# Optimization experiments

Measured on AMD Instinct MI355X. Metric: run time of the kernel, lower is better.

The kernel has to match this reference:

```python
import jax, jax.numpy as jnp
import numpy as np

S, E, K, D = 20000, 10000, 128, 128   # students, exercises, knowledge, latent dim
N_EK, N_SE = 40000, 500000            # exercise-knowledge edges, student-exercise edges
B = 2048                              # extract batch size


def setup_inputs() -> dict:
    key = jax.random.key(0)
    ks = jax.random.split(key, 16)
    inp = {}
    # Embedding tables (xavier-ish scale)
    inp["stu_emb"] = jax.random.normal(ks[0], (S, D), jnp.float32) * 0.1
    inp["exer_emb"] = jax.random.normal(ks[1], (E, D), jnp.float32) * 0.1
    inp["kn_emb"] = jax.random.normal(ks[2], (K, D), jnp.float32) * 0.1
    inp["disc_emb"] = jax.random.normal(ks[3], (E, 1), jnp.float32) * 0.1
    # GraphLayer params, stacked over [fusion_layer=2, graph={k_from_e,e_from_k,s_from_e,e_from_s}]
    inp["GW"] = jax.random.normal(ks[4], (2, 4, D, D), jnp.float32) * (1.0 / np.sqrt(D))
    inp["Ga"] = jax.random.normal(ks[5], (2, 4, 2 * D), jnp.float32) * 0.1
    # Fusion attention fcs: idx 0=e_attn_fc1, 1=e_attn_fc2, 2=k_attn_fc3 (weight [2D], bias scalar)
    inp["Fw"] = jax.random.normal(ks[6], (2, 3, 2 * D), jnp.float32) * 0.1
    inp["Fb"] = jax.random.normal(ks[7], (2, 3), jnp.float32) * 0.1
    # q_mask (unused by extract, part of the signature)
    inp["q_mask"] = jax.random.bernoulli(ks[8], 0.03, (B, K)).astype(jnp.float32)
    inp["student_id"] = jax.random.randint(ks[9], (B,), 0, S, jnp.int32)
    inp["exercise_id"] = jax.random.randint(ks[10], (B,), 0, E, jnp.int32)
    # k_from_e graph: nodes = [exercises 0..E) ++ [knowledge E..E+K); edges exercise -> knowledge
    inp["ek_src"] = jax.random.randint(ks[11], (N_EK,), 0, E, jnp.int32)
    inp["ek_dst"] = E + jax.random.randint(ks[12], (N_EK,), 0, K, jnp.int32)
    # s_from_e graph: nodes = [exercises 0..E) ++ [students E..E+S); edges exercise -> student
    inp["se_src"] = jax.random.randint(ks[13], (N_SE,), 0, E, jnp.int32)
    inp["se_dst"] = E + jax.random.randint(ks[14], (N_SE,), 0, S, jnp.int32)
    return inp


def _graph_layer(h, W, a, src, dst, n):
    # GAT-style: z = h W; per-edge score a^T [z_src; z_dst]; segment softmax over dst; weighted sum of z_src.
    z = h @ W                                   # [n, D]
    zs, zd = z[src], z[dst]                     # [ne, D] gathers
    e = jnp.concatenate([zs, zd], axis=1) @ a   # [ne]
    emax = jax.ops.segment_max(e, dst, num_segments=n)
    emax = jnp.where(jnp.isfinite(emax), emax, 0.0)  # empty segments -> -inf -> 0
    ex = jnp.exp(e - emax[dst])
    den = jax.ops.segment_sum(ex, dst, num_segments=n)
    alpha = ex / jnp.where(den > 0, den, 1.0)[dst]
    return jax.ops.segment_sum(alpha[:, None] * zs, dst, num_segments=n)  # nodes w/o mail -> 0 (DGL semantics)


def _fusion(kn, ex, st, GWl, Gal, Fwl, Fbl, ek_src, ek_dst, se_src, se_dst):
    nek, nes = E + K, E + S
    ekg = jnp.concatenate([ex, kn], axis=0)
    kfe = _graph_layer(ekg, GWl[0], Gal[0], ek_src, ek_dst, nek)  # k_from_e
    efk = _graph_layer(ekg, GWl[1], Gal[1], ek_dst, ek_src, nek)  # e_from_k (reversed edges)
    esg = jnp.concatenate([ex, st], axis=0)
    ufe = _graph_layer(esg, GWl[2], Gal[2], se_src, se_dst, nes)  # s_from_e
    efu = _graph_layer(esg, GWl[3], Gal[3], se_dst, se_src, nes)  # e_from_s (reversed edges)
    # knowledge update: softmax over a single column == 1 (faithful to original)
    Dk = kfe[E:]
    s3 = jax.nn.softmax((jnp.concatenate([kn, Dk], axis=1) @ Fwl[2] + Fbl[2])[:, None], axis=1)
    kn2 = kn + s3[:, 0:1] * Dk
    # exercise update: 2-way softmax gate
    Bx, Cx = efk[:E], efu[:E]
    s1 = jnp.concatenate([ex, Bx], axis=1) @ Fwl[0] + Fbl[0]
    s2 = jnp.concatenate([ex, Cx], axis=1) @ Fwl[1] + Fbl[1]
    sc = jax.nn.softmax(jnp.stack([s1, s2], axis=1), axis=1)  # [E, 2]
    ex2 = ex + sc[:, 0:1] * Bx + sc[:, 1:2] * Cx
    st2 = st + ufe[E:]
    return kn2, ex2, st2


def reference(stu_emb, exer_emb, kn_emb, disc_emb, GW, Ga, Fw, Fb, q_mask,
              student_id, exercise_id, ek_src, ek_dst, se_src, se_dst):
    kn, ex, st = kn_emb, exer_emb, stu_emb
    for l in range(2):  # FusionLayer1, FusionLayer2
        kn, ex, st = _fusion(kn, ex, st, GW[l], Ga[l], Fw[l], Fb[l],
                             ek_src, ek_dst, se_src, se_dst)
    bs = st[student_id]            # [B, D]
    be = ex[exercise_id]           # [B, D]
    disc = disc_emb[exercise_id]   # [B, 1]
    # if_type == 'rcd': repeat(1,D).reshape(B,D,D) == broadcast along axis 1
    stu_ts = jnp.broadcast_to(bs[:, None, :], (B, D, D))
    exer_ts = jnp.broadcast_to(be[:, None, :], (B, D, D))
    kn_ts = jnp.broadcast_to(kn[None, :, :], (B, K, D))
    return (stu_ts, exer_ts, disc, kn_ts)
```

## Files before the change

kernel.cpp:

```cpp
#include <hip/hip_runtime.h>

#define S_N 20000
#define E_N 10000
#define K_N 128
#define D_N 128
#define NEK 40000
#define NSE 500000
#define B_N 2048

typedef __attribute__((ext_vector_type(8))) short bf16x8;
typedef __attribute__((ext_vector_type(4))) float f32x4;

__device__ __forceinline__ unsigned short f2bf(float f){
  unsigned int u = __float_as_uint(f);
  unsigned int r = u + 0x7FFFu + ((u >> 16) & 1u);
  return (unsigned short)(r >> 16);
}
__device__ __forceinline__ float bf2f(unsigned short h){
  return __uint_as_float(((unsigned int)h) << 16);
}

struct GS { const unsigned short* Ah; const unsigned short* Al;
            const unsigned short* Wh; const unsigned short* Wl;
            float* Z; int rows; };
struct SSet { const float* z; const float* p; const int* rowptr; const int* col;
              const float* base; float* out; int ndst; };
struct CSet { const int* cnt; int n; int* rp; int* cur; };

__global__ __launch_bounds__(256) void k_wprep(const float* __restrict__ GW, const float* __restrict__ Ga,
                                               unsigned short* __restrict__ wf, float* __restrict__ wa){
  int g = blockIdx.x;
  const float* W  = GW + (size_t)g*16384;
  const float* a1 = Ga + (size_t)g*256;
  unsigned short* whi = wf + (size_t)g*16384;
  unsigned short* wlo = wf + (size_t)(8+g)*16384;
  int t = threadIdx.x, l = t & 63;
  for(int pi = t>>6; pi < 32; pi += 4){
    int c2 = pi >> 2, kt = pi & 3;
    unsigned short h[8], lo[8];
    #pragma unroll
    for(int j=0;j<8;j++){
      int k = kt*32 + (l>>4)*8 + j;
      int c = c2*16 + (l&15);
      float f = W[(size_t)k*128 + c];
      unsigned short hb = f2bf(f);
      h[j] = hb; lo[j] = f2bf(f - bf2f(hb));
    }
    size_t off = ((size_t)pi*64 + l)*8;
    uint4 hv, lv;
    hv.x = (unsigned)h[0] | ((unsigned)h[1]<<16);  hv.y = (unsigned)h[2] | ((unsigned)h[3]<<16);
    hv.z = (unsigned)h[4] | ((unsigned)h[5]<<16);  hv.w = (unsigned)h[6] | ((unsigned)h[7]<<16);
    lv.x = (unsigned)lo[0] | ((unsigned)lo[1]<<16); lv.y = (unsigned)lo[2] | ((unsigned)lo[3]<<16);
    lv.z = (unsigned)lo[4] | ((unsigned)lo[5]<<16); lv.w = (unsigned)lo[6] | ((unsigned)lo[7]<<16);
    *(uint4*)(whi + off) = hv;
    *(uint4*)(wlo + off) = lv;
  }
  for(int k = t; k < 128; k += 256){
    float s = 0.f;
    const float* wr = W + (size_t)k*128;
    for(int c=0;c<128;c++) s += wr[c]*a1[c];
    wa[(size_t)g*128 + k] = s;
  }
}

__global__ __launch_bounds__(256) void k_cvt(const float* __restrict__ kn, const float* __restrict__ ex,
    const float* __restrict__ st,
    unsigned short* __restrict__ knb, unsigned short* __restrict__ exb, unsigned short* __restrict__ stb,
    const float* __restrict__ wa, int l4,
    float* __restrict__ Pefk, float* __restrict__ Pkfe, float* __restrict__ Pufe, float* __restrict__ Pefu){
  int w = (blockIdx.x*256 + threadIdx.x) >> 6;
  int lane = threadIdx.x & 63;
  const float* src; unsigned short *hi, *lo; int r;
  const float* wv1; const float* wv2 = nullptr; float *P1, *P2 = nullptr;
  if(w < K_N){ r = w; src = kn + (size_t)r*128; hi = knb; lo = knb + (size_t)K_N*128;
               wv1 = wa + (size_t)(l4+1)*128; P1 = Pefk; }
  else if(w < K_N + E_N){ r = w - K_N; src = ex + (size_t)r*128; hi = exb; lo = exb + (size_t)E_N*128;
               wv1 = wa + (size_t)(l4+0)*128; P1 = Pkfe;
               wv2 = wa + (size_t)(l4+2)*128; P2 = Pufe; }
  else { r = w - K_N - E_N; if(r >= S_N) return; src = st + (size_t)r*128; hi = stb; lo = stb + (size_t)S_N*128;
               wv1 = wa + (size_t)(l4+3)*128; P1 = Pefu; }
  float2 x = ((const float2*)src)[lane];
  float2 v1 = ((const float2*)wv1)[lane];
  float d1 = x.x*v1.x + x.y*v1.y;
  float d2 = 0.f;
  if(wv2){ float2 v2 = ((const float2*)wv2)[lane]; d2 = x.x*v2.x + x.y*v2.y; }
  #pragma unroll
  for(int off=1; off<64; off<<=1){ d1 += __shfl_xor(d1,off); d2 += __shfl_xor(d2,off); }
  if(lane==0){ P1[r] = expf(d1); if(P2) P2[r] = expf(d2); }
  unsigned short h0 = f2bf(x.x), h1 = f2bf(x.y);
  unsigned short l0 = f2bf(x.x - bf2f(h0)), l1 = f2bf(x.y - bf2f(h1));
  ((ushort2*)(hi + (size_t)r*128))[lane] = make_ushort2(h0,h1);
  ((ushort2*)(lo + (size_t)r*128))[lane] = make_ushort2(l0,l1);
}

#define GT0 4
#define GT1 317
#define GT2 942
#define GT3 1255
__global__ __launch_bounds__(256) void k_gemm(GS g0, GS g1, GS g2, GS g3){
  int b = blockIdx.x;
  GS g; int lt;
  if(b < GT0){ g = g0; lt = b; }
  else if(b < GT1){ g = g1; lt = b - GT0; }
  else if(b < GT2){ g = g2; lt = b - GT1; }
  else { g = g3; lt = b - GT2; }
  int l = threadIdx.x & 63, wv = threadIdx.x >> 6;
  int r0 = lt*32;
  bf16x8 bh[2][4], bl[2][4];
  #pragma unroll
  for(int cs=0; cs<2; cs++)
    #pragma unroll
    for(int kt=0; kt<4; kt++){
      size_t o = (((size_t)((wv*2+cs)*4 + kt))*64 + l)*8;
      bh[cs][kt] = *(const bf16x8*)(g.Wh + o);
      bl[cs][kt] = *(const bf16x8*)(g.Wl + o);
    }
  f32x4 acc[2][2];
  #pragma unroll
  for(int rs=0;rs<2;rs++)
    #pragma unroll
    for(int cs=0;cs<2;cs++) acc[rs][cs] = (f32x4){0.f,0.f,0.f,0.f};
  #pragma unroll
  for(int kt=0; kt<4; kt++){
    bf16x8 ah[2], al[2];
    #pragma unroll
    for(int rs=0; rs<2; rs++){
      size_t ao = ((size_t)(r0 + rs*16 + (l&15)))*128 + kt*32 + (l>>4)*8;
      ah[rs] = *(const bf16x8*)(g.Ah + ao);
      al[rs] = *(const bf16x8*)(g.Al + ao);
    }
    #pragma unroll
    for(int rs=0; rs<2; rs++)
      #pragma unroll
      for(int cs=0; cs<2; cs++){
        acc[rs][cs] = __builtin_amdgcn_mfma_f32_16x16x32_bf16(ah[rs], bh[cs][kt], acc[rs][cs], 0,0,0);
        acc[rs][cs] = __builtin_amdgcn_mfma_f32_16x16x32_bf16(ah[rs], bl[cs][kt], acc[rs][cs], 0,0,0);
        acc[rs][cs] = __builtin_amdgcn_mfma_f32_16x16x32_bf16(al[rs], bh[cs][kt], acc[rs][cs], 0,0,0);
      }
  }
  #pragma unroll
  for(int rs=0; rs<2; rs++)
    #pragma unroll
    for(int cs=0; cs<2; cs++){
      int cb = (wv<<5) + (cs<<4) + (l&15);
      #pragma unroll
      for(int j=0;j<4;j++){
        int rr = r0 + rs*16 + ((l>>4)<<2) + j;
        if(rr < g.rows) g.Z[(size_t)rr*128 + cb] = acc[rs][cs][j];
      }
    }
}

__global__ __launch_bounds__(256) void k_hist(const int* __restrict__ eks, const int* __restrict__ ekd,
      const int* __restrict__ ses, const int* __restrict__ sed,
      int* c_eke, int* c_ekk, int* c_see, int* c_ses){
  int i = blockIdx.x*256 + threadIdx.x;
  if(i < NEK){ atomicAdd(c_eke + eks[i], 1); atomicAdd(c_ekk + (ekd[i]-E_N), 1); }
  if(i < NSE){ atomicAdd(c_see + ses[i], 1); atomicAdd(c_ses + (sed[i]-E_N), 1); }
}

__global__ __launch_bounds__(1024) void k_scan(CSet c0, CSet c1, CSet c2, CSet c3){
  CSet c = c0;
  if(blockIdx.x==1) c=c1; else if(blockIdx.x==2) c=c2; else if(blockIdx.x==3) c=c3;
  __shared__ int part[1024];
  int t = threadIdx.x;
  int n = c.n;
  int chunk = (n + 1023) >> 10;
  int b0 = t * chunk;
  int s = 0;
  for(int i=0;i<chunk;i++){ int idx=b0+i; if(idx<n) s += c.cnt[idx]; }
  part[t] = s;
  __syncthreads();
  for(int off=1; off<1024; off<<=1){
    int v = (t>=off) ? part[t-off] : 0;
    __syncthreads();
    part[t] += v;
    __syncthreads();
  }
  int run = t ? part[t-1] : 0;
  for(int i=0;i<chunk;i++){
    int idx=b0+i;
    if(idx<n){ int cc = c.cnt[idx]; c.rp[idx]=run; c.cur[idx]=run; run += cc; }
  }
  if(t==0) c.rp[n] = part[1023];
}

__global__ __launch_bounds__(256) void k_fill(const int* __restrict__ eks, const int* __restrict__ ekd,
      const int* __restrict__ ses, const int* __restrict__ sed,
      int* u_eke, int* u_ekk, int* u_see, int* u_ses,
      int* o_eke, int* o_ekk, int* o_see, int* o_ses){
  int i = blockIdx.x*256 + threadIdx.x;
  if(i < NEK){
    int a = eks[i], b = ekd[i];
    int pos = atomicAdd(u_eke + a, 1);        o_eke[pos] = b;
    int pos2 = atomicAdd(u_ekk + (b-E_N), 1); o_ekk[pos2] = a;
  }
  if(i < NSE){
    int a = ses[i], b = sed[i];
    int pos = atomicAdd(u_see + a, 1);        o_see[pos] = b;
    int pos2 = atomicAdd(u_ses + (b-E_N), 1); o_ses[pos2] = a;
  }
}

#define SB1 2500
#define SB2 5000
#define SB3 10000
#define SB4 10128
__global__ __launch_bounds__(256) void k_seg(SSet s0, SSet s1, SSet s2, SSet s3){
  __shared__ float4 red[4][32];
  __shared__ float redd[4];
  int b = blockIdx.x;
  int lane = threadIdx.x & 63, wid = threadIdx.x >> 6;
  int half = lane >> 5, l32 = lane & 31;
  SSet s; int row, str, stride; bool multi = false;
  if(b < SB1){ s = s0; row = b*4 + wid; }
  else if(b < SB2){ s = s1; row = (b-SB1)*4 + wid; }
  else if(b < SB3){ s = s2; row = (b-SB2)*4 + wid; }
  else { s = s3; row = b - SB3; multi = true; }
  if(!multi){ str = half; stride = 2; }
  else      { str = wid*2 + half; stride = 8; }
  if(row >= s.ndst) return;
  int e0 = s.rowptr[row], e1 = s.rowptr[row+1];
  const int* col = s.col; const float* p = s.p; const float* z = s.z;
  float4 acc = {0.f,0.f,0.f,0.f}; float den = 0.f;
  int e = e0 + str;
  for(; e + 3*stride < e1; e += 4*stride){
    int cA = col[e], cB = col[e+stride], cC = col[e+2*stride], cD = col[e+3*stride];
    float xA = p[cA], xB = p[cB], xC = p[cC], xD = p[cD];
    float4 zA = ((const float4*)(z + (size_t)cA*128))[l32];
    float4 zB = ((const float4*)(z + (size_t)cB*128))[l32];
    float4 zC = ((const float4*)(z + (size_t)cC*128))[l32];
    float4 zD = ((const float4*)(z + (size_t)cD*128))[l32];
    acc.x += xA*zA.x + xB*zB.x + xC*zC.x + xD*zD.x;
    acc.y += xA*zA.y + xB*zB.y + xC*zC.y + xD*zD.y;
    acc.z += xA*zA.z + xB*zB.z + xC*zC.z + xD*zD.z;
    acc.w += xA*zA.w + xB*zB.w + xC*zC.w + xD*zD.w;
    den += (xA + xB) + (xC + xD);
  }
  for(; e < e1; e += stride){
    int cA = col[e];
    float xA = p[cA];
    float4 zA = ((const float4*)(z + (size_t)cA*128))[l32];
    acc.x += xA*zA.x; acc.y += xA*zA.y; acc.z += xA*zA.z; acc.w += xA*zA.w;
    den += xA;
  }
  acc.x += __shfl_xor(acc.x,32); acc.y += __shfl_xor(acc.y,32);
  acc.z += __shfl_xor(acc.z,32); acc.w += __shfl_xor(acc.w,32);
  den   += __shfl_xor(den,32);
  if(multi){
    if(half==0){ red[wid][l32] = acc; if(l32==0) redd[wid] = den; }
    __syncthreads();
    if(wid) return;
    acc = red[0][l32]; den = redd[0];
    #pragma unroll
    for(int i=1;i<4;i++){
      float4 r4 = red[i][l32];
      acc.x+=r4.x; acc.y+=r4.y; acc.z+=r4.z; acc.w+=r4.w; den += redd[i];
    }
  }
  float inv = den > 0.f ? 1.f/den : 0.f;
  float4 res = {acc.x*inv, acc.y*inv, acc.z*inv, acc.w*inv};
  if(s.base){
    float4 b4 = ((const float4*)(s.base + (size_t)row*128))[l32];
    res.x+=b4.x; res.y+=b4.y; res.z+=b4.z; res.w+=b4.w;
  }
  if(half==0) ((float4*)(s.out + (size_t)row*128))[l32] = res;
}

__global__ __launch_bounds__(256) void k_exup(const float* __restrict__ base, float* __restrict__ ex,
     const float* __restrict__ Bx, const float* __restrict__ Cx,
     const float* __restrict__ Fw, const float* __restrict__ Fb){
  int w = (blockIdx.x*256 + threadIdx.x) >> 6;
  int lane = threadIdx.x & 63;
  if(w >= E_N) return;
  const float* er = base + (size_t)w*128;
  const float* br = Bx + (size_t)w*128;
  const float* cr = Cx + (size_t)w*128;
  float e0 = er[lane], e1 = er[lane+64];
  float b0 = br[lane], b1 = br[lane+64];
  float c0 = cr[lane], c1 = cr[lane+64];
  float s1 = e0*Fw[lane]     + e1*Fw[lane+64]
           + b0*Fw[lane+128] + b1*Fw[lane+192];
  float s2 = e0*Fw[256+lane]     + e1*Fw[256+lane+64]
           + c0*Fw[256+lane+128] + c1*Fw[256+lane+192];
  #pragma unroll
  for(int off=32; off; off>>=1){ s1 += __shfl_down(s1,off); s2 += __shfl_down(s2,off); }
  s1 = __shfl(s1, 0) + Fb[0];
  s2 = __shfl(s2, 0) + Fb[1];
  float mx = fmaxf(s1,s2);
  float pp = expf(s1-mx), qq = expf(s2-mx);
  float inv = 1.f/(pp+qq);
  float* orow = ex + (size_t)w*128;
  orow[lane]    = e0 + (pp*inv)*b0 + (qq*inv)*c0;
  orow[lane+64] = e1 + (pp*inv)*b1 + (qq*inv)*c1;
}

__global__ __launch_bounds__(256) void k_out(const float* __restrict__ st, const float* __restrict__ ex,
    const float* __restrict__ kn, const float* __restrict__ disc,
    const int* __restrict__ sid, const int* __restrict__ eid,
    float* out0, float* out1, float* out2, float* out3){
  int w = (blockIdx.x*256 + threadIdx.x) >> 6;
  int lane = threadIdx.x & 63;
  const int ROWW = 3*B_N*64;
  if(w < ROWW){
    int half = lane>>5, l32 = lane&31;
    int r = w*2 + half;
    int sec = r >> 18;
    int rr = r & 262143;
    int b = rr >> 7, i = rr & 127;
    const float* emb; int srow; float* ob;
    if(sec==0){ emb=st; srow=sid[b]; ob=out0; }
    else if(sec==1){ emb=ex; srow=eid[b]; ob=out1; }
    else { emb=kn; srow=i; ob=out3; }
    f32x4 v = *((const f32x4*)(emb + (size_t)srow*128) + l32);
    __builtin_nontemporal_store(v, (f32x4*)(ob + (size_t)rr*128) + l32);
  } else {
    int i = (w - ROWW)*64 + lane;
    if(i < B_N) out2[i] = disc[eid[i]];
  }
}

extern "C" void kernel_launch(void* const* d_in, const int* in_sizes, int n_in,
                              void* d_out, int out_size, void* d_ws, size_t ws_size,
                              hipStream_t stream){
  (void)in_sizes; (void)out_size; (void)ws_size;
  const float* stu_emb  = (const float*)d_in[0];
  const float* exer_emb = (const float*)d_in[1];
  const float* kn_emb   = (const float*)d_in[2];
  const float* disc_emb = (const float*)d_in[3];
  const float* GW = (const float*)d_in[4];
  const float* Ga = (const float*)d_in[5];
  const float* Fw = (const float*)d_in[6];
  const float* Fb = (const float*)d_in[7];
  int base = n_in - 6;
  const int* sid    = (const int*)d_in[base];
  const int* eid    = (const int*)d_in[base+1];
  const int* ek_src = (const int*)d_in[base+2];
  const int* ek_dst = (const int*)d_in[base+3];
  const int* se_src = (const int*)d_in[base+4];
  const int* se_dst = (const int*)d_in[base+5];

  char* w = (char*)d_ws;
  size_t off = 0;
  auto alloc = [&](size_t bytes)->char*{ char* p = w + off; off += (bytes + 255) & ~(size_t)255; return p; };
  float* st_f = (float*)alloc((size_t)S_N*D_N*4);
  float* ex_f = (float*)alloc((size_t)E_N*D_N*4);
  float* kn_f = (float*)alloc((size_t)K_N*D_N*4);
  float* Bx   = (float*)alloc((size_t)E_N*D_N*4);
  float* Cx   = (float*)alloc((size_t)E_N*D_N*4);
  float* zefk = (float*)alloc((size_t)K_N*D_N*4);
  float* zkfe = (float*)alloc((size_t)E_N*D_N*4);
  float* zefu = (float*)alloc((size_t)S_N*D_N*4);
  float* zufe = (float*)alloc((size_t)E_N*D_N*4);
  float* Pefk = (float*)alloc((size_t)K_N*4);
  float* Pkfe = (float*)alloc((size_t)E_N*4);
  float* Pefu = (float*)alloc((size_t)S_N*4);
  float* Pufe = (float*)alloc((size_t)E_N*4);
  unsigned short* knb = (unsigned short*)alloc((size_t)K_N*D_N*2*2 + 4096);
  unsigned short* exb = (unsigned short*)alloc((size_t)E_N*D_N*2*2 + 4096);
  unsigned short* stb = (unsigned short*)alloc((size_t)S_N*D_N*2*2 + 4096);
  unsigned short* wf  = (unsigned short*)alloc((size_t)16*16384*2);
  float* wa   = (float*)alloc((size_t)8*128*4);
  int*   cnt  = (int*)alloc((size_t)(2*E_N+K_N+S_N)*4);
  int*   rp   = (int*)alloc((size_t)(2*(E_N+1)+(K_N+1)+(S_N+1))*4);
  int*   cur  = (int*)alloc((size_t)(2*E_N+K_N+S_N)*4);
  int*   col  = (int*)alloc((size_t)(2*NEK+2*NSE)*4);

  int* cnt_eke = cnt;                 int* cnt_ekk = cnt + E_N;
  int* cnt_see = cnt + E_N + K_N;     int* cnt_ses = cnt + 2*E_N + K_N;
  int* cur_eke = cur;                 int* cur_ekk = cur + E_N;
  int* cur_see = cur + E_N + K_N;     int* cur_ses = cur + 2*E_N + K_N;
  int* rp_eke = rp;                                int* rp_ekk = rp + (E_N+1);
  int* rp_see = rp + (E_N+1) + (K_N+1);            int* rp_ses = rp + 2*(E_N+1) + (K_N+1);
  int* col_eke = col;                 int* col_ekk = col + NEK;
  int* col_see = col + 2*NEK;         int* col_ses = col + 2*NEK + NSE;

  hipMemsetAsync(cnt, 0, (size_t)(2*E_N+K_N+S_N)*4, stream);
  k_wprep<<<8,256,0,stream>>>(GW, Ga, wf, wa);
  const int gb = (NSE+255)/256;
  k_hist<<<gb,256,0,stream>>>(ek_src, ek_dst, se_src, se_dst, cnt_eke, cnt_ekk, cnt_see, cnt_ses);
  k_scan<<<4,1024,0,stream>>>(CSet{cnt_eke,E_N,rp_eke,cur_eke}, CSet{cnt_ekk,K_N,rp_ekk,cur_ekk},
                              CSet{cnt_see,E_N,rp_see,cur_see}, CSet{cnt_ses,S_N,rp_ses,cur_ses});
  k_fill<<<gb,256,0,stream>>>(ek_src, ek_dst, se_src, se_dst,
                              cur_eke, cur_ekk, cur_see, cur_ses,
                              col_eke, col_ekk, col_see, col_ses);

  const unsigned short* knb_lo = knb + (size_t)K_N*128;
  const unsigned short* exb_lo = exb + (size_t)E_N*128;
  const unsigned short* stb_lo = stb + (size_t)S_N*128;

  for(int l=0; l<2; l++){
    const float* knp = l ? kn_f : kn_emb;
    const float* exp_ = l ? ex_f : exer_emb;
    const float* stp = l ? st_f : stu_emb;
    int l4 = l*4;
    k_cvt<<<(K_N+E_N+S_N)/4,256,0,stream>>>(knp, exp_, stp, knb, exb, stb, wa, l4,
                                            Pefk, Pkfe, Pufe, Pefu);
    GS g0{knb, knb_lo, wf + (size_t)(l4+1)*16384, wf + (size_t)(8+l4+1)*16384, zefk, K_N};
    GS g1{exb, exb_lo, wf + (size_t)(l4+0)*16384, wf + (size_t)(8+l4+0)*16384, zkfe, E_N};
    GS g2{stb, stb_lo, wf + (size_t)(l4+3)*16384, wf + (size_t)(8+l4+3)*16384, zefu, S_N};
    GS g3{exb, exb_lo, wf + (size_t)(l4+2)*16384, wf + (size_t)(8+l4+2)*16384, zufe, E_N};
    k_gemm<<<GT3,256,0,stream>>>(g0,g1,g2,g3);
    SSet s0{zefk - (size_t)E_N*128, Pefk - E_N, rp_eke, col_eke, nullptr, Bx,   E_N};
    SSet s1{zefu - (size_t)E_N*128, Pefu - E_N, rp_see, col_see, nullptr, Cx,   E_N};
    SSet s2{zufe,                   Pufe,       rp_ses, col_ses, stp,     st_f, S_N};
    SSet s3{zkfe,                   Pkfe,       rp_ekk, col_ekk, knp,     kn_f, K_N};
    k_seg<<<SB4,256,0,stream>>>(s0,s1,s2,s3);
    k_exup<<<(E_N*64)/256,256,0,stream>>>(exp_, ex_f, Bx, Cx, Fw + (size_t)l*3*2*D_N, Fb + (size_t)l*3);
  }

  float* out  = (float*)d_out;
  float* out0 = out;
  float* out1 = out0 + (size_t)B_N*D_N*D_N;
  float* out2 = out1 + (size_t)B_N*D_N*D_N;
  float* out3 = out2 + (size_t)B_N;
  int waves = 3*B_N*64 + 32;
  k_out<<<(waves+3)/4,256,0,stream>>>(st_f, ex_f, kn_f, disc_emb, sid, eid, out0, out1, out2, out3);
}
```

Measured before the change: 798.5 us.

## Fuse exercise gate update into segment aggregation and merge weight prep into histogram

The exercise-side segment softmax sums for the knowledge and student graphs are now computed by the same wave, which then applies the two-way attention gate directly. This removes the Bx/Cx intermediate buffers and the separate k_exup launch each layer. The weight preparation kernel is folded into the histogram kernel as extra blocks, saving one launch. Each exercise wave now performs two gathers in sequence, so per-block work is less balanced and fewer blocks are launched overall.

```diff
diff --git a/kernel.cpp b/kernel.cpp
--- a/kernel.cpp
+++ b/kernel.cpp
@@ -23,43 +23,95 @@
 struct GS { const unsigned short* Ah; const unsigned short* Al;
             const unsigned short* Wh; const unsigned short* Wl;
             float* Z; int rows; };
-struct SSet { const float* z; const float* p; const int* rowptr; const int* col;
-              const float* base; float* out; int ndst; };
 struct CSet { const int* cnt; int n; int* rp; int* cur; };
 
-__global__ __launch_bounds__(256) void k_wprep(const float* __restrict__ GW, const float* __restrict__ Ga,
-                                               unsigned short* __restrict__ wf, float* __restrict__ wa){
-  int g = blockIdx.x;
-  const float* W  = GW + (size_t)g*16384;
-  const float* a1 = Ga + (size_t)g*256;
-  unsigned short* whi = wf + (size_t)g*16384;
-  unsigned short* wlo = wf + (size_t)(8+g)*16384;
-  int t = threadIdx.x, l = t & 63;
-  for(int pi = t>>6; pi < 32; pi += 4){
-    int c2 = pi >> 2, kt = pi & 3;
-    unsigned short h[8], lo[8];
-    #pragma unroll
-    for(int j=0;j<8;j++){
-      int k = kt*32 + (l>>4)*8 + j;
-      int c = c2*16 + (l&15);
-      float f = W[(size_t)k*128 + c];
-      unsigned short hb = f2bf(f);
-      h[j] = hb; lo[j] = f2bf(f - bf2f(hb));
-    }
-    size_t off = ((size_t)pi*64 + l)*8;
-    uint4 hv, lv;
-    hv.x = (unsigned)h[0] | ((unsigned)h[1]<<16);  hv.y = (unsigned)h[2] | ((unsigned)h[3]<<16);
-    hv.z = (unsigned)h[4] | ((unsigned)h[5]<<16);  hv.w = (unsigned)h[6] | ((unsigned)h[7]<<16);
-    lv.x = (unsigned)lo[0] | ((unsigned)lo[1]<<16); lv.y = (unsigned)lo[2] | ((unsigned)lo[3]<<16);
-    lv.z = (unsigned)lo[4] | ((unsigned)lo[5]<<16); lv.w = (unsigned)lo[6] | ((unsigned)lo[7]<<16);
-    *(uint4*)(whi + off) = hv;
-    *(uint4*)(wlo + off) = lv;
-  }
-  for(int k = t; k < 128; k += 256){
-    float s = 0.f;
-    const float* wr = W + (size_t)k*128;
-    for(int c=0;c<128;c++) s += wr[c]*a1[c];
-    wa[(size_t)g*128 + k] = s;
+#define HB ((NSE+255)/256)
+__global__ __launch_bounds__(256) void k_hist(const int* __restrict__ eks, const int* __restrict__ ekd,
+      const int* __restrict__ ses, const int* __restrict__ sed,
+      int* c_eke, int* c_ekk, int* c_see, int* c_ses,
+      const float* __restrict__ GW, const float* __restrict__ Ga,
+      unsigned short* __restrict__ wf, float* __restrict__ wa){
+  int bb = blockIdx.x;
+  if(bb >= HB){
+    int g = bb - HB;
+    const float* W  = GW + (size_t)g*16384;
+    const float* a1 = Ga + (size_t)g*256;
+    unsigned short* whi = wf + (size_t)g*16384;
+    unsigned short* wlo = wf + (size_t)(8+g)*16384;
+    int t = threadIdx.x, l = t & 63;
+    for(int pi = t>>6; pi < 32; pi += 4){
+      int c2 = pi >> 2, kt = pi & 3;
+      unsigned short h[8], lo[8];
+      #pragma unroll
+      for(int j=0;j<8;j++){
+        int k = kt*32 + (l>>4)*8 + j;
+        int c = c2*16 + (l&15);
+        float f = W[(size_t)k*128 + c];
+        unsigned short hb = f2bf(f);
+        h[j] = hb; lo[j] = f2bf(f - bf2f(hb));
+      }
+      size_t off = ((size_t)pi*64 + l)*8;
+      uint4 hv, lv;
+      hv.x = (unsigned)h[0] | ((unsigned)h[1]<<16);  hv.y = (unsigned)h[2] | ((unsigned)h[3]<<16);
+      hv.z = (unsigned)h[4] | ((unsigned)h[5]<<16);  hv.w = (unsigned)h[6] | ((unsigned)h[7]<<16);
+      lv.x = (unsigned)lo[0] | ((unsigned)lo[1]<<16); lv.y = (unsigned)lo[2] | ((unsigned)lo[3]<<16);
+      lv.z = (unsigned)lo[4] | ((unsigned)lo[5]<<16); lv.w = (unsigned)lo[6] | ((unsigned)lo[7]<<16);
+      *(uint4*)(whi + off) = hv;
+      *(uint4*)(wlo + off) = lv;
+    }
+    for(int k = t; k < 128; k += 256){
+      float s = 0.f;
+      const float* wr = W + (size_t)k*128;
+      for(int c=0;c<128;c++) s += wr[c]*a1[c];
+      wa[(size_t)g*128 + k] = s;
+    }
+    return;
+  }
+  int i = bb*256 + threadIdx.x;
+  if(i < NEK){ atomicAdd(c_eke + eks[i], 1); atomicAdd(c_ekk + (ekd[i]-E_N), 1); }
+  if(i < NSE){ atomicAdd(c_see + ses[i], 1); atomicAdd(c_ses + (sed[i]-E_N), 1); }
+}
+
+__global__ __launch_bounds__(1024) void k_scan(CSet c0, CSet c1, CSet c2, CSet c3){
+  CSet c = c0;
+  if(blockIdx.x==1) c=c1; else if(blockIdx.x==2) c=c2; else if(blockIdx.x==3) c=c3;
+  __shared__ int part[1024];
+  int t = threadIdx.x;
+  int n = c.n;
+  int chunk = (n + 1023) >> 10;
+  int b0 = t * chunk;
+  int s = 0;
+  for(int i=0;i<chunk;i++){ int idx=b0+i; if(idx<n) s += c.cnt[idx]; }
+  part[t] = s;
+  __syncthreads();
+  for(int off=1; off<1024; off<<=1){
+    int v = (t>=off) ? part[t-off] : 0;
+    __syncthreads();
+    part[t] += v;
+    __syncthreads();
+  }
+  int run = t ? part[t-1] : 0;
+  for(int i=0;i<chunk;i++){
+    int idx=b0+i;
+    if(idx<n){ int cc = c.cnt[idx]; c.rp[idx]=run; c.cur[idx]=run; run += cc; }
+  }
+  if(t==0) c.rp[n] = part[1023];
+}
+
+__global__ __launch_bounds__(256) void k_fill(const int* __restrict__ eks, const int* __restrict__ ekd,
+      const int* __restrict__ ses, const int* __restrict__ sed,
+      int* u_eke, int* u_ekk, int* u_see, int* u_ses,
+      int* o_eke, int* o_ekk, int* o_see, int* o_ses){
+  int i = blockIdx.x*256 + threadIdx.x;
+  if(i < NEK){
+    int a = eks[i], b = ekd[i];
+    int pos = atomicAdd(u_eke + a, 1);        o_eke[pos] = b;
+    int pos2 = atomicAdd(u_ekk + (b-E_N), 1); o_ekk[pos2] = a;
+  }
+  if(i < NSE){
+    int a = ses[i], b = sed[i];
+    int pos = atomicAdd(u_see + a, 1);        o_see[pos] = b;
+    int pos2 = atomicAdd(u_ses + (b-E_N), 1); o_ses[pos2] = a;
   }
 }
 
@@ -151,81 +203,13 @@
     }
 }
 
-__global__ __launch_bounds__(256) void k_hist(const int* __restrict__ eks, const int* __restrict__ ekd,
-      const int* __restrict__ ses, const int* __restrict__ sed,
-      int* c_eke, int* c_ekk, int* c_see, int* c_ses){
-  int i = blockIdx.x*256 + threadIdx.x;
-  if(i < NEK){ atomicAdd(c_eke + eks[i], 1); atomicAdd(c_ekk + (ekd[i]-E_N), 1); }
-  if(i < NSE){ atomicAdd(c_see + ses[i], 1); atomicAdd(c_ses + (sed[i]-E_N), 1); }
-}
-
-__global__ __launch_bounds__(1024) void k_scan(CSet c0, CSet c1, CSet c2, CSet c3){
-  CSet c = c0;
-  if(blockIdx.x==1) c=c1; else if(blockIdx.x==2) c=c2; else if(blockIdx.x==3) c=c3;
-  __shared__ int part[1024];
-  int t = threadIdx.x;
-  int n = c.n;
-  int chunk = (n + 1023) >> 10;
-  int b0 = t * chunk;
-  int s = 0;
-  for(int i=0;i<chunk;i++){ int idx=b0+i; if(idx<n) s += c.cnt[idx]; }
-  part[t] = s;
-  __syncthreads();
-  for(int off=1; off<1024; off<<=1){
-    int v = (t>=off) ? part[t-off] : 0;
-    __syncthreads();
-    part[t] += v;
-    __syncthreads();
-  }
-  int run = t ? part[t-1] : 0;
-  for(int i=0;i<chunk;i++){
-    int idx=b0+i;
-    if(idx<n){ int cc = c.cnt[idx]; c.rp[idx]=run; c.cur[idx]=run; run += cc; }
-  }
-  if(t==0) c.rp[n] = part[1023];
-}
-
-__global__ __launch_bounds__(256) void k_fill(const int* __restrict__ eks, const int* __restrict__ ekd,
-      const int* __restrict__ ses, const int* __restrict__ sed,
-      int* u_eke, int* u_ekk, int* u_see, int* u_ses,
-      int* o_eke, int* o_ekk, int* o_see, int* o_ses){
-  int i = blockIdx.x*256 + threadIdx.x;
-  if(i < NEK){
-    int a = eks[i], b = ekd[i];
-    int pos = atomicAdd(u_eke + a, 1);        o_eke[pos] = b;
-    int pos2 = atomicAdd(u_ekk + (b-E_N), 1); o_ekk[pos2] = a;
-  }
-  if(i < NSE){
-    int a = ses[i], b = sed[i];
-    int pos = atomicAdd(u_see + a, 1);        o_see[pos] = b;
-    int pos2 = atomicAdd(u_ses + (b-E_N), 1); o_ses[pos2] = a;
-  }
-}
-
-#define SB1 2500
-#define SB2 5000
-#define SB3 10000
-#define SB4 10128
-__global__ __launch_bounds__(256) void k_seg(SSet s0, SSet s1, SSet s2, SSet s3){
-  __shared__ float4 red[4][32];
-  __shared__ float redd[4];
-  int b = blockIdx.x;
-  int lane = threadIdx.x & 63, wid = threadIdx.x >> 6;
-  int half = lane >> 5, l32 = lane & 31;
-  SSet s; int row, str, stride; bool multi = false;
-  if(b < SB1){ s = s0; row = b*4 + wid; }
-  else if(b < SB2){ s = s1; row = (b-SB1)*4 + wid; }
-  else if(b < SB3){ s = s2; row = (b-SB2)*4 + wid; }
-  else { s = s3; row = b - SB3; multi = true; }
-  if(!multi){ str = half; stride = 2; }
-  else      { str = wid*2 + half; stride = 8; }
-  if(row >= s.ndst) return;
-  int e0 = s.rowptr[row], e1 = s.rowptr[row+1];
-  const int* col = s.col; const float* p = s.p; const float* z = s.z;
+__device__ __forceinline__ void seg_row(const float* __restrict__ z, const float* __restrict__ p,
+                                        const int* __restrict__ col, int e0, int e1,
+                                        int half, int l32, float4& accO, float& denO){
   float4 acc = {0.f,0.f,0.f,0.f}; float den = 0.f;
-  int e = e0 + str;
-  for(; e + 3*stride < e1; e += 4*stride){
-    int cA = col[e], cB = col[e+stride], cC = col[e+2*stride], cD = col[e+3*stride];
+  int e = e0 + half;
+  for(; e + 6 < e1; e += 8){
+    int cA = col[e], cB = col[e+2], cC = col[e+4], cD = col[e+6];
     float xA = p[cA], xB = p[cB], xC = p[cC], xD = p[cD];
     float4 zA = ((const float4*)(z + (size_t)cA*128))[l32];
     float4 zB = ((const float4*)(z + (size_t)cB*128))[l32];
@@ -237,7 +221,7 @@
     acc.w += xA*zA.w + xB*zB.w + xC*zC.w + xD*zD.w;
     den += (xA + xB) + (xC + xD);
   }
-  for(; e < e1; e += stride){
+  for(; e < e1; e += 2){
     int cA = col[e];
     float xA = p[cA];
     float4 zA = ((const float4*)(z + (size_t)cA*128))[l32];
@@ -247,7 +231,92 @@
   acc.x += __shfl_xor(acc.x,32); acc.y += __shfl_xor(acc.y,32);
   acc.z += __shfl_xor(acc.z,32); acc.w += __shfl_xor(acc.w,32);
   den   += __shfl_xor(den,32);
-  if(multi){
+  accO = acc; denO = den;
+}
+
+#define S2A 2500
+#define S2B 7500
+#define S2C 7628
+__global__ __launch_bounds__(256) void k_seg2(
+    const float* __restrict__ zB, const float* __restrict__ pB, const int* __restrict__ rpB, const int* __restrict__ colB,
+    const float* __restrict__ zC, const float* __restrict__ pC, const int* __restrict__ rpC, const int* __restrict__ colC,
+    const float* __restrict__ zS, const float* __restrict__ pS, const int* __restrict__ rpS, const int* __restrict__ colS,
+    const float* __restrict__ stBase, float* __restrict__ stOut,
+    const float* __restrict__ zK, const float* __restrict__ pK, const int* __restrict__ rpK, const int* __restrict__ colK,
+    const float* __restrict__ knBase, float* __restrict__ knOut,
+    const float* __restrict__ exBase, float* __restrict__ exOut,
+    const float* __restrict__ Fwl, const float* __restrict__ Fbl){
+  __shared__ float4 red[4][32];
+  __shared__ float redd[4];
+  int b = blockIdx.x;
+  int lane = threadIdx.x & 63, wid = threadIdx.x >> 6;
+  int half = lane >> 5, l32 = lane & 31;
+  if(b < S2A){
+    int row = b*4 + wid;
+    float4 accB; float denB;
+    seg_row(zB, pB, colB, rpB[row], rpB[row+1], half, l32, accB, denB);
+    float4 accC; float denC;
+    seg_row(zC, pC, colC, rpC[row], rpC[row+1], half, l32, accC, denC);
+    float invB = denB > 0.f ? 1.f/denB : 0.f;
+    float invC = denC > 0.f ? 1.f/denC : 0.f;
+    float4 Bx4 = {accB.x*invB, accB.y*invB, accB.z*invB, accB.w*invB};
+    float4 Cx4 = {accC.x*invC, accC.y*invC, accC.z*invC, accC.w*invC};
+    float4 ex4 = ((const float4*)(exBase + (size_t)row*128))[l32];
+    float4 fa = *(const float4*)(Fwl + 4*l32);
+    float4 fb = *(const float4*)(Fwl + 128 + 4*l32);
+    float4 fc = *(const float4*)(Fwl + 256 + 4*l32);
+    float4 fd = *(const float4*)(Fwl + 384 + 4*l32);
+    float s1 = ex4.x*fa.x + ex4.y*fa.y + ex4.z*fa.z + ex4.w*fa.w
+             + Bx4.x*fb.x + Bx4.y*fb.y + Bx4.z*fb.z + Bx4.w*fb.w;
+    float s2 = ex4.x*fc.x + ex4.y*fc.y + ex4.z*fc.z + ex4.w*fc.w
+             + Cx4.x*fd.x + Cx4.y*fd.y + Cx4.z*fd.z + Cx4.w*fd.w;
+    #pragma unroll
+    for(int off=1; off<32; off<<=1){ s1 += __shfl_xor(s1,off); s2 += __shfl_xor(s2,off); }
+    s1 += Fbl[0]; s2 += Fbl[1];
+    float mx = fmaxf(s1,s2);
+    float pp = expf(s1-mx), qq = expf(s2-mx);
+    float iv = 1.f/(pp+qq);
+    pp *= iv; qq *= iv;
+    float4 o = {ex4.x + pp*Bx4.x + qq*Cx4.x, ex4.y + pp*Bx4.y + qq*Cx4.y,
+                ex4.z + pp*Bx4.z + qq*Cx4.z, ex4.w + pp*Bx4.w + qq*Cx4.w};
+    if(half==0) ((float4*)(exOut + (size_t)row*128))[l32] = o;
+  } else if(b < S2B){
+    int row = (b-S2A)*4 + wid;
+    float4 acc; float den;
+    seg_row(zS, pS, colS, rpS[row], rpS[row+1], half, l32, acc, den);
+    float inv = den > 0.f ? 1.f/den : 0.f;
+    float4 b4 = ((const float4*)(stBase + (size_t)row*128))[l32];
+    float4 res = {acc.x*inv + b4.x, acc.y*inv + b4.y, acc.z*inv + b4.z, acc.w*inv + b4.w};
+    if(half==0) ((float4*)(stOut + (size_t)row*128))[l32] = res;
+  } else {
+    int row = b - S2B;
+    int e0 = rpK[row], e1 = rpK[row+1];
+    float4 acc = {0.f,0.f,0.f,0.f}; float den = 0.f;
+    int str = wid*2 + half;
+    int e = e0 + str;
+    for(; e + 24 < e1; e += 32){
+      int cA = colK[e], cB = colK[e+8], cC = colK[e+16], cD = colK[e+24];
+      float xA = pK[cA], xB = pK[cB], xC = pK[cC], xD = pK[cD];
+      float4 zA = ((const float4*)(zK + (size_t)cA*128))[l32];
+      float4 zB4 = ((const float4*)(zK + (size_t)cB*128))[l32];
+      float4 zC4 = ((const float4*)(zK + (size_t)cC*128))[l32];
+      float4 zD4 = ((const float4*)(zK + (size_t)cD*128))[l32];
+      acc.x += xA*zA.x + xB*zB4.x + xC*zC4.x + xD*zD4.x;
+      acc.y += xA*zA.y + xB*zB4.y + xC*zC4.y + xD*zD4.y;
+      acc.z += xA*zA.z + xB*zB4.z + xC*zC4.z + xD*zD4.z;
+      acc.w += xA*zA.w + xB*zB4.w + xC*zC4.w + xD*zD4.w;
+      den += (xA + xB) + (xC + xD);
+    }
+    for(; e < e1; e += 8){
+      int cA = colK[e];
+      float xA = pK[cA];
+      float4 zA = ((const float4*)(zK + (size_t)cA*128))[l32];
+      acc.x += xA*zA.x; acc.y += xA*zA.y; acc.z += xA*zA.z; acc.w += xA*zA.w;
+      den += xA;
+    }
+    acc.x += __shfl_xor(acc.x,32); acc.y += __shfl_xor(acc.y,32);
+    acc.z += __shfl_xor(acc.z,32); acc.w += __shfl_xor(acc.w,32);
+    den   += __shfl_xor(den,32);
     if(half==0){ red[wid][l32] = acc; if(l32==0) redd[wid] = den; }
     __syncthreads();
     if(wid) return;
@@ -257,42 +326,11 @@
       float4 r4 = red[i][l32];
       acc.x+=r4.x; acc.y+=r4.y; acc.z+=r4.z; acc.w+=r4.w; den += redd[i];
     }
-  }
-  float inv = den > 0.f ? 1.f/den : 0.f;
-  float4 res = {acc.x*inv, acc.y*inv, acc.z*inv, acc.w*inv};
-  if(s.base){
-    float4 b4 = ((const float4*)(s.base + (size_t)row*128))[l32];
-    res.x+=b4.x; res.y+=b4.y; res.z+=b4.z; res.w+=b4.w;
-  }
-  if(half==0) ((float4*)(s.out + (size_t)row*128))[l32] = res;
-}
-
-__global__ __launch_bounds__(256) void k_exup(const float* __restrict__ base, float* __restrict__ ex,
-     const float* __restrict__ Bx, const float* __restrict__ Cx,
-     const float* __restrict__ Fw, const float* __restrict__ Fb){
-  int w = (blockIdx.x*256 + threadIdx.x) >> 6;
-  int lane = threadIdx.x & 63;
-  if(w >= E_N) return;
-  const float* er = base + (size_t)w*128;
-  const float* br = Bx + (size_t)w*128;
-  const float* cr = Cx + (size_t)w*128;
-  float e0 = er[lane], e1 = er[lane+64];
-  float b0 = br[lane], b1 = br[lane+64];
-  float c0 = cr[lane], c1 = cr[lane+64];
-  float s1 = e0*Fw[lane]     + e1*Fw[lane+64]
-           + b0*Fw[lane+128] + b1*Fw[lane+192];
-  float s2 = e0*Fw[256+lane]     + e1*Fw[256+lane+64]
-           + c0*Fw[256+lane+128] + c1*Fw[256+lane+192];
-  #pragma unroll
-  for(int off=32; off; off>>=1){ s1 += __shfl_down(s1,off); s2 += __shfl_down(s2,off); }
-  s1 = __shfl(s1, 0) + Fb[0];
-  s2 = __shfl(s2, 0) + Fb[1];
-  float mx = fmaxf(s1,s2);
-  float pp = expf(s1-mx), qq = expf(s2-mx);
-  float inv = 1.f/(pp+qq);
-  float* orow = ex + (size_t)w*128;
-  orow[lane]    = e0 + (pp*inv)*b0 + (qq*inv)*c0;
-  orow[lane+64] = e1 + (pp*inv)*b1 + (qq*inv)*c1;
+    float inv = den > 0.f ? 1.f/den : 0.f;
+    float4 b4 = ((const float4*)(knBase + (size_t)row*128))[l32];
+    float4 res = {acc.x*inv + b4.x, acc.y*inv + b4.y, acc.z*inv + b4.z, acc.w*inv + b4.w};
+    if(half==0) ((float4*)(knOut + (size_t)row*128))[l32] = res;
+  }
 }
 
 __global__ __launch_bounds__(256) void k_out(const float* __restrict__ st, const float* __restrict__ ex,
@@ -346,8 +384,6 @@
   float* st_f = (float*)alloc((size_t)S_N*D_N*4);
   float* ex_f = (float*)alloc((size_t)E_N*D_N*4);
   float* kn_f = (float*)alloc((size_t)K_N*D_N*4);
-  float* Bx   = (float*)alloc((size_t)E_N*D_N*4);
-  float* Cx   = (float*)alloc((size_t)E_N*D_N*4);
   float* zefk = (float*)alloc((size_t)K_N*D_N*4);
   float* zkfe = (float*)alloc((size_t)E_N*D_N*4);
   float* zefu = (float*)alloc((size_t)S_N*D_N*4);
@@ -376,12 +412,12 @@
   int* col_see = col + 2*NEK;         int* col_ses = col + 2*NEK + NSE;
 
   hipMemsetAsync(cnt, 0, (size_t)(2*E_N+K_N+S_N)*4, stream);
-  k_wprep<<<8,256,0,stream>>>(GW, Ga, wf, wa);
-  const int gb = (NSE+255)/256;
-  k_hist<<<gb,256,0,stream>>>(ek_src, ek_dst, se_src, se_dst, cnt_eke, cnt_ekk, cnt_see, cnt_ses);
+  k_hist<<<HB+8,256,0,stream>>>(ek_src, ek_dst, se_src, se_dst,
+                                cnt_eke, cnt_ekk, cnt_see, cnt_ses,
+                                GW, Ga, wf, wa);
   k_scan<<<4,1024,0,stream>>>(CSet{cnt_eke,E_N,rp_eke,cur_eke}, CSet{cnt_ekk,K_N,rp_ekk,cur_ekk},
                               CSet{cnt_see,E_N,rp_see,cur_see}, CSet{cnt_ses,S_N,rp_ses,cur_ses});
-  k_fill<<<gb,256,0,stream>>>(ek_src, ek_dst, se_src, se_dst,
+  k_fill<<<HB,256,0,stream>>>(ek_src, ek_dst, se_src, se_dst,
                               cur_eke, cur_ekk, cur_see, cur_ses,
                               col_eke, col_ekk, col_see, col_ses);
 
@@ -401,12 +437,12 @@
     GS g2{stb, stb_lo, wf + (size_t)(l4+3)*16384, wf + (size_t)(8+l4+3)*16384, zefu, S_N};
     GS g3{exb, exb_lo, wf + (size_t)(l4+2)*16384, wf + (size_t)(8+l4+2)*16384, zufe, E_N};
     k_gemm<<<GT3,256,0,stream>>>(g0,g1,g2,g3);
-    SSet s0{zefk - (size_t)E_N*128, Pefk - E_N, rp_eke, col_eke, nullptr, Bx,   E_N};
-    SSet s1{zefu - (size_t)E_N*128, Pefu - E_N, rp_see, col_see, nullptr, Cx,   E_N};
-    SSet s2{zufe,                   Pufe,       rp_ses, col_ses, stp,     st_f, S_N};
-    SSet s3{zkfe,                   Pkfe,       rp_ekk, col_ekk, knp,     kn_f, K_N};
-    k_seg<<<SB4,256,0,stream>>>(s0,s1,s2,s3);
-    k_exup<<<(E_N*64)/256,256,0,stream>>>(exp_, ex_f, Bx, Cx, Fw + (size_t)l*3*2*D_N, Fb + (size_t)l*3);
+    k_seg2<<<S2C,256,0,stream>>>(
+      zefk - (size_t)E_N*128, Pefk - E_N, rp_eke, col_eke,
+      zefu - (size_t)E_N*128, Pefu - E_N, rp_see, col_see,
+      zufe, Pufe, rp_ses, col_ses, stp, st_f,
+      zkfe, Pkfe, rp_ekk, col_ekk, knp, kn_f,
+      exp_, ex_f, Fw + (size_t)l*3*2*D_N, Fb + (size_t)l*3);
   }
 
   float* out  = (float*)d_out;
```

New measurement: 775.0 us. -2.9%, faster.
